# Kernel optimization log

Measured on AMD Instinct MI355X. Metric: run time of the kernel, lower is better.

Reference implementation:

```python
import jax, jax.numpy as jnp
import numpy as np

D_MODEL = 2048
N_HEADS = 16
HEAD_DIM = D_MODEL // N_HEADS  # 128
BASE = 10000.0
NEG = -1e9


def _rope_tables(seq_len, dtype=jnp.float32):
    # inv_freq over even dims of head_dim, emb = cat(freqs, freqs)
    inv_freq = 1.0 / (BASE ** (jnp.arange(0, HEAD_DIM, 2, dtype=jnp.float32) / HEAD_DIM))
    t = jnp.arange(seq_len, dtype=jnp.float32)
    freqs = jnp.einsum('i,j->ij', t, inv_freq)          # [S, hd/2]
    emb = jnp.concatenate([freqs, freqs], axis=-1)       # [S, hd]
    return jnp.cos(emb).astype(dtype)[None, None], jnp.sin(emb).astype(dtype)[None, None]


def _rotate_half(x):
    # Faithful to source: rotary_ndims == head_dim, so x2 is empty and this returns x.
    x1, x2 = x[..., :HEAD_DIM], x[..., HEAD_DIM:]
    return jnp.concatenate([-x2, x1], axis=-1)


def setup_inputs() -> dict:
    key = jax.random.key(0)
    ks = jax.random.split(key, 5)
    B, S = 2, 2048
    x = jax.random.normal(ks[0], (B, S, D_MODEL), dtype=jnp.float32)
    # additive causal mask [1,1,S,S]
    causal = jnp.tril(jnp.ones((S, S), dtype=bool))
    attention_mask = jnp.where(causal, 0.0, NEG).astype(jnp.float32)[None, None]
    scale = 1.0 / np.sqrt(D_MODEL)
    Wq = jax.random.normal(ks[1], (D_MODEL, D_MODEL), dtype=jnp.float32) * scale
    Wk = jax.random.normal(ks[2], (D_MODEL, D_MODEL), dtype=jnp.float32) * scale
    Wv = jax.random.normal(ks[3], (D_MODEL, D_MODEL), dtype=jnp.float32) * scale
    Wd = jax.random.normal(ks[4], (D_MODEL, D_MODEL), dtype=jnp.float32) * scale
    return {"x": x, "attention_mask": attention_mask, "Wq": Wq, "Wk": Wk, "Wv": Wv, "Wd": Wd}


def reference(x, attention_mask, Wq, Wk, Wv, Wd):
    B, S, _ = x.shape
    # torch Linear: y = x @ W.T  (weights stored [out, in])
    def proj(W):
        y = jnp.einsum('bsd,ed->bse', x, W)
        return y.reshape(B, S, N_HEADS, HEAD_DIM).transpose(0, 2, 1, 3)  # [B,H,S,hd]
    q, k, v = proj(Wq), proj(Wk), proj(Wv)
    cos, sin = _rope_tables(S, x.dtype)
    q = q * cos + _rotate_half(q) * sin
    k = k * cos + _rotate_half(k) * sin
    scores = jnp.einsum('bhqd,bhkd->bhqk', q, k) / jnp.sqrt(jnp.float32(HEAD_DIM)).astype(x.dtype)
    scores = scores + attention_mask
    attn = jax.nn.softmax(scores, axis=-1)
    out = jnp.einsum('bhqk,bhkd->bhqd', attn, v)
    out = out.transpose(0, 2, 1, 3).reshape(B, S, D_MODEL)
    return jnp.einsum('bse,de->bsd', out, Wd)
```

## Files before the change

### kernel.cpp

```cpp
#include <hip/hip_runtime.h>
#include <stdint.h>

#define DM   2048
#define NH   16
#define HD   128
#define BB   2
#define SS   2048
#define MM   (BB*SS)
#define KK   2048
#define NQKV (3*DM)

#define LOG2E  1.4426950408889634f
#define SCALE  0.08838834764831845f

using bf16x8 = __attribute__((ext_vector_type(8))) __bf16;
using f32x4  = __attribute__((ext_vector_type(4))) float;
typedef unsigned short u16;
typedef unsigned int   u32;

__device__ __forceinline__ u16 f2bf(float f) {
  u32 u = __float_as_uint(f);
  u32 r = (u + 0x7FFFu + ((u >> 16) & 1u)) >> 16;
  return (u16)r;
}

__device__ __forceinline__ void load_lds16(const void* g, void* l) {
  __builtin_amdgcn_global_load_lds(
      (__attribute__((address_space(1))) void*)(g),
      (__attribute__((address_space(3))) void*)(l), 16, 0, 0);
}

__global__ void cast_f32_bf16(const float* __restrict__ s, u16* __restrict__ d, int n) {
  int i = (blockIdx.x * blockDim.x + threadIdx.x) * 4;
  if (i < n) {
    float4 f = *(const float4*)(s + i);
    u32 lo = (u32)f2bf(f.x) | ((u32)f2bf(f.y) << 16);
    u32 hi = (u32)f2bf(f.z) | ((u32)f2bf(f.w) << 16);
    *(uint2*)(d + i) = make_uint2(lo, hi);
  }
}

__global__ void rope_fct(float* __restrict__ f) {
  int i = blockIdx.x * blockDim.x + threadIdx.x;
  if (i < SS * 128) {
    int s = i >> 7, j = i & 127;
    double inv = pow(10000.0, -(double)(j & 63) / 64.0);
    float ang = (float)s * (float)inv;
    float sn, cs;
    sincosf(ang, &sn, &cs);
    f[i] = cs + sn;
  }
}


__device__ __forceinline__ void stage_unit(const u16* __restrict__ G, int rowbase,
                                           int kbase, u16* lds, int tid) {
#pragma unroll
  for (int i = 0; i < 2; i++) {
    int s = i * 512 + tid;
    int r = s >> 3, c = s & 7;
    load_lds16(G + (size_t)(rowbase + r) * KK + kbase + ((c ^ (r & 7)) * 8),
               (char*)lds + (size_t)s * 16);
  }
}

#define GEMM_MAIN_LOOP(EXTRA_LAST)                                              \
  const int tid = threadIdx.x;                                                  \
  const int wid = tid >> 6, lane = tid & 63, ln = lane & 15, quad = lane >> 4;  \
  const int wm = wid >> 2, wn = wid & 3;                                        \
  const int m0 = blockIdx.x * 256, n0 = blockIdx.y * 128;                       \
  const f32x4 fz = {0.f, 0.f, 0.f, 0.f};                                        \
  f32x4 acc[8][2];                                                              \
  _Pragma("unroll") for (int mi = 0; mi < 8; mi++)                              \
    _Pragma("unroll") for (int ni = 0; ni < 2; ni++) acc[mi][ni] = fz;          \
  int aRow[8], bRow[2];                                                         \
  _Pragma("unroll") for (int mi = 0; mi < 8; mi++)                              \
    aRow[mi] = ((mi < 4) ? (wm * 64 + mi * 16)                                  \
                         : (128 + wm * 64 + (mi - 4) * 16)) + ln;               \
  _Pragma("unroll") for (int ni = 0; ni < 2; ni++)                              \
    bRow[ni] = wn * 32 + ni * 16 + ln;                                          \
                        \
  stage_unit(Bm, n0, 0, LB[0], tid);                                            \
  stage_unit(A, m0, 0, LA[0], tid);                                             \
  stage_unit(A, m0 + 128, 0, LA[0] + 128 * 64, tid);                            \
  const int nT = KK / 64;                                                       \
  for (int t = 0; t < nT; t++) {                                                \
    const int cur = t & 1;                                                      \
    const u16* At = LA[cur];                                                    \
    const u16* Bt = LB[cur];                                                    \
    u16* Ax = LA[cur ^ 1];                                                      \
    u16* Bx = LB[cur ^ 1];                                                      \
    const int kn = (t + 1) * 64;                                                \
    const bool nl = (t + 1 < nT);                                               \
    bf16x8 aF[2][4], bF[2][2];                                                  \
                                    \
    __asm__ __volatile__("s_waitcnt vmcnt(2)" ::: "memory");                    \
    __asm__ __volatile__("s_barrier" ::: "memory");                             \
    _Pragma("unroll") for (int kk = 0; kk < 2; kk++) {                          \
      _Pragma("unroll") for (int mi = 0; mi < 4; mi++)                          \
        aF[kk][mi] = *(const bf16x8*)&At[aRow[mi] * 64 +                        \
                      (((kk * 4 + quad) ^ (aRow[mi] & 7)) * 8)];                \
      _Pragma("unroll") for (int ni = 0; ni < 2; ni++)                          \
        bF[kk][ni] = *(const bf16x8*)&Bt[bRow[ni] * 64 +                        \
                      (((kk * 4 + quad) ^ (bRow[ni] & 7)) * 8)];                \
    }                                                                           \
    if (nl) stage_unit(Bm, n0, kn, Bx, tid);                                    \
    __asm__ __volatile__("s_waitcnt lgkmcnt(0)" ::: "memory");                  \
    __builtin_amdgcn_sched_barrier(0);                                          \
    __builtin_amdgcn_s_setprio(1);                                              \
    _Pragma("unroll") for (int kk = 0; kk < 2; kk++)                            \
      _Pragma("unroll") for (int mi = 0; mi < 4; mi++)                          \
        _Pragma("unroll") for (int ni = 0; ni < 2; ni++)                        \
          acc[mi][ni] = __builtin_amdgcn_mfma_f32_16x16x32_bf16(                \
              aF[kk][mi], bF[kk][ni], acc[mi][ni], 0, 0, 0);                    \
    __builtin_amdgcn_s_setprio(0);                                              \
    __builtin_amdgcn_sched_barrier(0);                                          \
                                  \
    if (nl) { __asm__ __volatile__("s_waitcnt vmcnt(2)" ::: "memory"); }        \
    else    { __asm__ __volatile__("s_waitcnt vmcnt(0)" ::: "memory"); }        \
    __asm__ __volatile__("s_barrier" ::: "memory");                             \
    _Pragma("unroll") for (int kk = 0; kk < 2; kk++)                            \
      _Pragma("unroll") for (int mi = 0; mi < 4; mi++)                          \
        aF[kk][mi] = *(const bf16x8*)&At[aRow[4 + mi] * 64 +                    \
                      (((kk * 4 + quad) ^ (aRow[4 + mi] & 7)) * 8)];            \
    if (nl) {                                                                   \
      stage_unit(A, m0, kn, Ax, tid);                                           \
      stage_unit(A, m0 + 128, kn, Ax + 128 * 64, tid);                          \
    }                                                                           \
    __asm__ __volatile__("s_waitcnt lgkmcnt(0)" ::: "memory");                  \
    __builtin_amdgcn_sched_barrier(0);                                          \
    __builtin_amdgcn_s_setprio(1);                                              \
    _Pragma("unroll") for (int kk = 0; kk < 2; kk++)                            \
      _Pragma("unroll") for (int mi = 0; mi < 4; mi++)                          \
        _Pragma("unroll") for (int ni = 0; ni < 2; ni++)                        \
          acc[4 + mi][ni] = __builtin_amdgcn_mfma_f32_16x16x32_bf16(            \
              aF[kk][mi], bF[kk][ni], acc[4 + mi][ni], 0, 0, 0);                \
    __builtin_amdgcn_s_setprio(0);                                              \
    __builtin_amdgcn_sched_barrier(0);                                          \
    (void)0; EXTRA_LAST                                                         \
  }

__global__ __launch_bounds__(512, 2)
void gemm_qkv_rope(const u16* __restrict__ A, const u16* __restrict__ Bm,
                   u16* __restrict__ qo, u16* __restrict__ ko, u16* __restrict__ vo,
                   const float* __restrict__ fct) {
  __shared__ __align__(16) u16 LA[2][256 * 64];
  __shared__ __align__(16) u16 LB[2][128 * 64];
  GEMM_MAIN_LOOP()

  const int tensor = n0 >> 11;
  const int h = (n0 & 2047) >> 7;
  if (tensor < 2) {
    u16* dst = (tensor == 0) ? qo : ko;
#pragma unroll
    for (int mi = 0; mi < 8; mi++) {
      int rowM = (mi < 4) ? (wm * 64 + mi * 16) : (128 + wm * 64 + (mi - 4) * 16);
#pragma unroll
      for (int r = 0; r < 4; r++) {
        int m = m0 + rowM + quad * 4 + r;
        int b = m >> 11, s = m & 2047;
        const float* fr = fct + s * 128;
#pragma unroll
        for (int ni = 0; ni < 2; ni++) {
          int j = wn * 32 + ni * 16 + ln;
          dst[((size_t)(b * NH + h) * SS + s) * HD + j] = f2bf(acc[mi][ni][r] * fr[j]);
        }
      }
    }
  } else {
    __syncthreads();
    u16* Tr = (u16*)LA;
    const int b = m0 >> 11, s0 = m0 & 2047;
#pragma unroll
    for (int mi = 0; mi < 8; mi++) {
      int rowM = (mi < 4) ? (wm * 64 + mi * 16) : (128 + wm * 64 + (mi - 4) * 16);
#pragma unroll
      for (int ni = 0; ni < 2; ni++) {
        int hd = wn * 32 + ni * 16 + ln;
#pragma unroll
        for (int r = 0; r < 4; r++) {
          int srel = rowM + quad * 4 + r;
          int ch = srel >> 3;
          Tr[hd * 256 + ((ch ^ (hd & 31)) * 8) + (srel & 7)] = f2bf(acc[mi][ni][r]);
        }
      }
    }
    __syncthreads();
#pragma unroll
    for (int it = 0; it < 8; it++) {
      int slot = it * 512 + tid;
      int hd = slot >> 5, c8 = slot & 31;
      uint4 val = *(const uint4*)&Tr[hd * 256 + ((c8 ^ (hd & 31)) * 8)];
      *(uint4*)(vo + ((size_t)(b * NH + h) * HD + hd) * SS + s0 + c8 * 8) = val;
    }
  }
}

__global__ __launch_bounds__(512, 2)
void gemm_out(const u16* __restrict__ A, const u16* __restrict__ Bm,
              float* __restrict__ C) {
  __shared__ __align__(16) u16 LA[2][256 * 64];
  __shared__ __align__(16) u16 LB[2][128 * 64];
  GEMM_MAIN_LOOP()

#pragma unroll
  for (int mi = 0; mi < 8; mi++) {
    int rowM = (mi < 4) ? (wm * 64 + mi * 16) : (128 + wm * 64 + (mi - 4) * 16);
#pragma unroll
    for (int r = 0; r < 4; r++) {
      int m = m0 + rowM + quad * 4 + r;
#pragma unroll
      for (int ni = 0; ni < 2; ni++)
        C[(size_t)m * DM + n0 + wn * 32 + ni * 16 + ln] = acc[mi][ni][r];
    }
  }
}

__global__ __launch_bounds__(256, 2)
void flash_attn(const u16* __restrict__ q, const u16* __restrict__ k,
                const u16* __restrict__ v, u16* __restrict__ o) {
  __shared__ __align__(16) u16 Ps[64 * 64];
  __shared__ __align__(16) u16 Ks[2][64 * 128];
  __shared__ __align__(16) u16 Vs[2][128 * 64];
  const int tid = threadIdx.x;
  const int w = tid >> 6, lane = tid & 63, ln = lane & 15, quad = lane >> 4;
  const int hh = blockIdx.y, b = blockIdx.z;
  const size_t bh = (size_t)b * NH + hh;
  const u16* Kg = k + bh * SS * HD;
  const u16* Vg = v + bh * HD * SS;

  for (int half = 0; half < 2; half++) {
    const int T = half ? (31 - (int)blockIdx.x) : (int)blockIdx.x;
    const u16* Qg = q + bh * SS * HD + (size_t)T * 64 * HD;

    bf16x8 qf[4];
#pragma unroll
    for (int kc = 0; kc < 4; kc++)
      qf[kc] = *(const bf16x8*)(Qg + (size_t)(w * 16 + ln) * HD + (kc * 4 + quad) * 8);

    __syncthreads();

#pragma unroll
    for (int i = 0; i < 4; i++) {
      int slot = i * 256 + tid;
      int r = slot >> 4, c = (slot & 15) ^ (r & 7);
      load_lds16(Kg + (size_t)r * HD + c * 8, (char*)Ks[0] + slot * 16);
    }
#pragma unroll
    for (int i = 0; i < 4; i++) {
      int slot = i * 256 + tid;
      int r = slot >> 3, c = (slot & 7) ^ (r & 7);
      load_lds16(Vg + (size_t)r * SS + c * 8, (char*)Vs[0] + slot * 16);
    }

    const f32x4 fz = {0.f, 0.f, 0.f, 0.f};
    float m_s[4], l_s[4];
    f32x4 accO[8];
#pragma unroll
    for (int r = 0; r < 4; r++) { m_s[r] = -1e30f; l_s[r] = 0.f; }
#pragma unroll
    for (int nt = 0; nt < 8; nt++) accO[nt] = fz;

    const int nkt = T + 1;
    const int qrb = T * 64 + w * 16;

    for (int kt = 0; kt < nkt; kt++) {
      const int cur = kt & 1;
      const int k0 = kt * 64;
      __asm__ __volatile__("s_waitcnt vmcnt(0)" ::: "memory");
      __syncthreads();
      if (kt + 1 < nkt) {
        const int kn = k0 + 64;
#pragma unroll
        for (int i = 0; i < 4; i++) {
          int slot = i * 256 + tid;
          int r = slot >> 4, c = (slot & 15) ^ (r & 7);
          load_lds16(Kg + (size_t)(kn + r) * HD + c * 8, (char*)Ks[cur ^ 1] + slot * 16);
        }
#pragma unroll
        for (int i = 0; i < 4; i++) {
          int slot = i * 256 + tid;
          int r = slot >> 3, c = (slot & 7) ^ (r & 7);
          load_lds16(Vg + (size_t)r * SS + kn + c * 8, (char*)Vs[cur ^ 1] + slot * 16);
        }
      }

      f32x4 sc[4];
#pragma unroll
      for (int nt = 0; nt < 4; nt++) sc[nt] = fz;
#pragma unroll
      for (int kc = 0; kc < 4; kc++)
#pragma unroll
        for (int nt = 0; nt < 4; nt++) {
          bf16x8 bf = *(const bf16x8*)&Ks[cur][(nt * 16 + ln) * 128 + (((kc * 4 + quad) ^ (ln & 7)) * 8)];
          sc[nt] = __builtin_amdgcn_mfma_f32_16x16x32_bf16(qf[kc], bf, sc[nt], 0, 0, 0);
        }

      const bool partial = (kt == T);
#pragma unroll
      for (int nt = 0; nt < 4; nt++)
#pragma unroll
        for (int r = 0; r < 4; r++) {
          float val = sc[nt][r] * SCALE;
          if (partial && (k0 + nt * 16 + ln > qrb + quad * 4 + r)) val = -1e9f;
          sc[nt][r] = val;
        }

#pragma unroll
      for (int r = 0; r < 4; r++) {
        float mx = fmaxf(fmaxf(sc[0][r], sc[1][r]), fmaxf(sc[2][r], sc[3][r]));
#pragma unroll
        for (int off = 1; off < 16; off <<= 1) mx = fmaxf(mx, __shfl_xor(mx, off));
        float mnew = fmaxf(m_s[r], mx);
        float alpha = exp2f((m_s[r] - mnew) * LOG2E);
        float rs = 0.f;
#pragma unroll
        for (int nt = 0; nt < 4; nt++) {
          float p = exp2f((sc[nt][r] - mnew) * LOG2E);
          sc[nt][r] = p;
          rs += p;
        }
#pragma unroll
        for (int off = 1; off < 16; off <<= 1) rs += __shfl_xor(rs, off);
        l_s[r] = l_s[r] * alpha + rs;
        m_s[r] = mnew;
#pragma unroll
        for (int nt = 0; nt < 8; nt++) accO[nt][r] *= alpha;
      }

#pragma unroll
      for (int nt = 0; nt < 4; nt++)
#pragma unroll
        for (int r = 0; r < 4; r++) {
          int rr = w * 16 + quad * 4 + r;
          int j = nt * 16 + ln;
          Ps[rr * 64 + (((j >> 3) ^ (rr & 7)) * 8) + (j & 7)] = f2bf(sc[nt][r]);
        }
      __asm__ __volatile__("s_waitcnt lgkmcnt(0)" ::: "memory");

      bf16x8 pf[2];
#pragma unroll
      for (int kc = 0; kc < 2; kc++) {
        int rp = w * 16 + ln;
        pf[kc] = *(const bf16x8*)&Ps[rp * 64 + (((kc * 4 + quad) ^ (ln & 7)) * 8)];
      }

#pragma unroll
      for (int kc = 0; kc < 2; kc++)
#pragma unroll
        for (int nt = 0; nt < 8; nt++) {
          bf16x8 vf = *(const bf16x8*)&Vs[cur][(nt * 16 + ln) * 64 + (((kc * 4 + quad) ^ (ln & 7)) * 8)];
          accO[nt] = __builtin_amdgcn_mfma_f32_16x16x32_bf16(pf[kc], vf, accO[nt], 0, 0, 0);
        }
    }

#pragma unroll
    for (int r = 0; r < 4; r++) {
      float ilv = 1.f / l_s[r];
      int srow = T * 64 + w * 16 + quad * 4 + r;
      size_t base = ((size_t)b * SS + srow) * DM + hh * HD;
#pragma unroll
      for (int nt = 0; nt < 8; nt++)
        o[base + nt * 16 + ln] = f2bf(accO[nt][r] * ilv);
    }
  }
}

extern "C" void kernel_launch(void* const* d_in, const int* in_sizes, int n_in,
                              void* d_out, int out_size, void* d_ws, size_t ws_size,
                              hipStream_t stream) {
  (void)in_sizes; (void)n_in; (void)out_size; (void)ws_size;
  const float* x  = (const float*)d_in[0];
  const float* Wq = (const float*)d_in[2];
  const float* Wk = (const float*)d_in[3];
  const float* Wv = (const float*)d_in[4];
  const float* Wd = (const float*)d_in[5];

  char* ws = (char*)d_ws;
  u16* xb   = (u16*)(ws);
  u16* aob  = xb;
  u16* wqkv = (u16*)(ws + 16777216ull);
  float* fct = (float*)(ws + 41943040ull);
  u16* wdb  = (u16*)(ws + 41943040ull);
  u16* qb   = (u16*)(ws + 50331648ull);
  u16* kb   = (u16*)(ws + 67108864ull);
  u16* vtb  = (u16*)(ws + 83886080ull);

  cast_f32_bf16<<<8192, 256, 0, stream>>>(x,  xb, MM * KK);
  cast_f32_bf16<<<4096, 256, 0, stream>>>(Wq, wqkv,                   DM * KK);
  cast_f32_bf16<<<4096, 256, 0, stream>>>(Wk, wqkv + (size_t)DM*KK,   DM * KK);
  cast_f32_bf16<<<4096, 256, 0, stream>>>(Wv, wqkv + (size_t)2*DM*KK, DM * KK);
  rope_fct<<<1024, 256, 0, stream>>>(fct);

  gemm_qkv_rope<<<dim3(MM / 256, NQKV / 128), 512, 0, stream>>>(xb, wqkv, qb, kb, vtb, fct);

  cast_f32_bf16<<<4096, 256, 0, stream>>>(Wd, wdb, DM * KK);

  flash_attn<<<dim3(16, NH, BB), 256, 0, stream>>>(qb, kb, vtb, aob);
  gemm_out<<<dim3(MM / 256, DM / 128), 512, 0, stream>>>(aob, wdb, (float*)d_out);
}
```

Before: 400.9 us.

## Transpose GEMM block tile to 128x256 with split B-staging pipeline

Switches the shared GEMM macro from a 256(M)x128(N) block tile to 128(M)x256(N), so each block covers two heads of output columns. LDS is repacked into one flat buffer, and the half-step pipeline now splits the B tile instead of the A tile, with the wait counts adjusted to match. The QKV epilogue gains per-column head indexing, and the V transpose path uses a new swizzle. The tile area and LDS footprint stay the same; the intent is a different stage/compute interleaving and wider output rows, at the risk of changed global load balance and wait-count correctness.

New measurement: 391.0 us. 1.03x faster.

```diff
diff --git a/kernel.cpp b/kernel.cpp
--- a/kernel.cpp
+++ b/kernel.cpp
@@ -64,36 +64,37 @@
   }
 }
 
-#define GEMM_MAIN_LOOP(EXTRA_LAST)                                              \
+#define COLN(ni) (((ni) < 2) ? (wn * 32 + (ni) * 16) : (128 + wn * 32 + ((ni) - 2) * 16))
+
+#define GEMM_MAIN_LOOP                                                          \
   const int tid = threadIdx.x;                                                  \
   const int wid = tid >> 6, lane = tid & 63, ln = lane & 15, quad = lane >> 4;  \
   const int wm = wid >> 2, wn = wid & 3;                                        \
-  const int m0 = blockIdx.x * 256, n0 = blockIdx.y * 128;                       \
+  const int m0 = blockIdx.x * 128, n0 = blockIdx.y * 256;                       \
   const f32x4 fz = {0.f, 0.f, 0.f, 0.f};                                        \
-  f32x4 acc[8][2];                                                              \
-  _Pragma("unroll") for (int mi = 0; mi < 8; mi++)                              \
-    _Pragma("unroll") for (int ni = 0; ni < 2; ni++) acc[mi][ni] = fz;          \
-  int aRow[8], bRow[2];                                                         \
-  _Pragma("unroll") for (int mi = 0; mi < 8; mi++)                              \
-    aRow[mi] = ((mi < 4) ? (wm * 64 + mi * 16)                                  \
-                         : (128 + wm * 64 + (mi - 4) * 16)) + ln;               \
-  _Pragma("unroll") for (int ni = 0; ni < 2; ni++)                              \
-    bRow[ni] = wn * 32 + ni * 16 + ln;                                          \
-                        \
-  stage_unit(Bm, n0, 0, LB[0], tid);                                            \
-  stage_unit(A, m0, 0, LA[0], tid);                                             \
-  stage_unit(A, m0 + 128, 0, LA[0] + 128 * 64, tid);                            \
+  f32x4 acc[4][4];                                                              \
+  _Pragma("unroll") for (int mi = 0; mi < 4; mi++)                              \
+    _Pragma("unroll") for (int ni = 0; ni < 4; ni++) acc[mi][ni] = fz;          \
+  int aRow[4], bRow[4];                                                         \
+  _Pragma("unroll") for (int mi = 0; mi < 4; mi++)                              \
+    aRow[mi] = wm * 64 + mi * 16 + ln;                                          \
+  _Pragma("unroll") for (int ni = 0; ni < 4; ni++)                              \
+    bRow[ni] = COLN(ni) + ln;                                                   \
+                            \
+  stage_unit(A, m0, 0, Sh, tid);                                                \
+  stage_unit(Bm, n0, 0, Sh + 16384, tid);                                       \
+  stage_unit(Bm, n0 + 128, 0, Sh + 16384 + 8192, tid);                          \
   const int nT = KK / 64;                                                       \
   for (int t = 0; t < nT; t++) {                                                \
     const int cur = t & 1;                                                      \
-    const u16* At = LA[cur];                                                    \
-    const u16* Bt = LB[cur];                                                    \
-    u16* Ax = LA[cur ^ 1];                                                      \
-    u16* Bx = LB[cur ^ 1];                                                      \
+    const u16* At = Sh + cur * 8192;                                            \
+    const u16* Bt = Sh + 16384 + cur * 16384;                                   \
+    u16* Ax = Sh + (cur ^ 1) * 8192;                                            \
+    u16* Bx = Sh + 16384 + (cur ^ 1) * 16384;                                   \
     const int kn = (t + 1) * 64;                                                \
     const bool nl = (t + 1 < nT);                                               \
     bf16x8 aF[2][4], bF[2][2];                                                  \
-                                    \
+                              \
     __asm__ __volatile__("s_waitcnt vmcnt(2)" ::: "memory");                    \
     __asm__ __volatile__("s_barrier" ::: "memory");                             \
     _Pragma("unroll") for (int kk = 0; kk < 2; kk++) {                          \
@@ -104,7 +105,10 @@
         bF[kk][ni] = *(const bf16x8*)&Bt[bRow[ni] * 64 +                        \
                       (((kk * 4 + quad) ^ (bRow[ni] & 7)) * 8)];                \
     }                                                                           \
-    if (nl) stage_unit(Bm, n0, kn, Bx, tid);                                    \
+    if (nl) {                                                                   \
+      stage_unit(A, m0, kn, Ax, tid);                                           \
+      stage_unit(Bm, n0, kn, Bx, tid);                                          \
+    }                                                                           \
     __asm__ __volatile__("s_waitcnt lgkmcnt(0)" ::: "memory");                  \
     __builtin_amdgcn_sched_barrier(0);                                          \
     __builtin_amdgcn_s_setprio(1);                                              \
@@ -115,73 +119,70 @@
               aF[kk][mi], bF[kk][ni], acc[mi][ni], 0, 0, 0);                    \
     __builtin_amdgcn_s_setprio(0);                                              \
     __builtin_amdgcn_sched_barrier(0);                                          \
-                                  \
-    if (nl) { __asm__ __volatile__("s_waitcnt vmcnt(2)" ::: "memory"); }        \
+                         \
+    if (nl) { __asm__ __volatile__("s_waitcnt vmcnt(4)" ::: "memory"); }        \
     else    { __asm__ __volatile__("s_waitcnt vmcnt(0)" ::: "memory"); }        \
     __asm__ __volatile__("s_barrier" ::: "memory");                             \
     _Pragma("unroll") for (int kk = 0; kk < 2; kk++)                            \
-      _Pragma("unroll") for (int mi = 0; mi < 4; mi++)                          \
-        aF[kk][mi] = *(const bf16x8*)&At[aRow[4 + mi] * 64 +                    \
-                      (((kk * 4 + quad) ^ (aRow[4 + mi] & 7)) * 8)];            \
-    if (nl) {                                                                   \
-      stage_unit(A, m0, kn, Ax, tid);                                           \
-      stage_unit(A, m0 + 128, kn, Ax + 128 * 64, tid);                          \
-    }                                                                           \
+      _Pragma("unroll") for (int ni = 0; ni < 2; ni++)                          \
+        bF[kk][ni] = *(const bf16x8*)&Bt[bRow[2 + ni] * 64 +                    \
+                      (((kk * 4 + quad) ^ (bRow[2 + ni] & 7)) * 8)];            \
+    if (nl) stage_unit(Bm, n0 + 128, kn, Bx + 8192, tid);                       \
     __asm__ __volatile__("s_waitcnt lgkmcnt(0)" ::: "memory");                  \
     __builtin_amdgcn_sched_barrier(0);                                          \
     __builtin_amdgcn_s_setprio(1);                                              \
     _Pragma("unroll") for (int kk = 0; kk < 2; kk++)                            \
       _Pragma("unroll") for (int mi = 0; mi < 4; mi++)                          \
         _Pragma("unroll") for (int ni = 0; ni < 2; ni++)                        \
-          acc[4 + mi][ni] = __builtin_amdgcn_mfma_f32_16x16x32_bf16(            \
-              aF[kk][mi], bF[kk][ni], acc[4 + mi][ni], 0, 0, 0);                \
+          acc[mi][2 + ni] = __builtin_amdgcn_mfma_f32_16x16x32_bf16(            \
+              aF[kk][mi], bF[kk][ni], acc[mi][2 + ni], 0, 0, 0);                \
     __builtin_amdgcn_s_setprio(0);                                              \
     __builtin_amdgcn_sched_barrier(0);                                          \
-    (void)0; EXTRA_LAST                                                         \
   }
 
 __global__ __launch_bounds__(512, 2)
 void gemm_qkv_rope(const u16* __restrict__ A, const u16* __restrict__ Bm,
                    u16* __restrict__ qo, u16* __restrict__ ko, u16* __restrict__ vo,
                    const float* __restrict__ fct) {
-  __shared__ __align__(16) u16 LA[2][256 * 64];
-  __shared__ __align__(16) u16 LB[2][128 * 64];
-  GEMM_MAIN_LOOP()
+  __shared__ __align__(16) u16 Sh[49152];
+  GEMM_MAIN_LOOP
 
   const int tensor = n0 >> 11;
-  const int h = (n0 & 2047) >> 7;
+  const int h0 = (n0 & 2047) >> 7;
   if (tensor < 2) {
     u16* dst = (tensor == 0) ? qo : ko;
 #pragma unroll
-    for (int mi = 0; mi < 8; mi++) {
-      int rowM = (mi < 4) ? (wm * 64 + mi * 16) : (128 + wm * 64 + (mi - 4) * 16);
+    for (int mi = 0; mi < 4; mi++) {
+      int rowM = wm * 64 + mi * 16;
 #pragma unroll
       for (int r = 0; r < 4; r++) {
         int m = m0 + rowM + quad * 4 + r;
         int b = m >> 11, s = m & 2047;
         const float* fr = fct + s * 128;
 #pragma unroll
-        for (int ni = 0; ni < 2; ni++) {
-          int j = wn * 32 + ni * 16 + ln;
+        for (int ni = 0; ni < 4; ni++) {
+          int colN = COLN(ni) + ln;
+          int h = h0 + (colN >> 7);
+          int j = colN & 127;
           dst[((size_t)(b * NH + h) * SS + s) * HD + j] = f2bf(acc[mi][ni][r] * fr[j]);
         }
       }
     }
   } else {
     __syncthreads();
-    u16* Tr = (u16*)LA;
+    u16* Tr = Sh;
     const int b = m0 >> 11, s0 = m0 & 2047;
 #pragma unroll
-    for (int mi = 0; mi < 8; mi++) {
-      int rowM = (mi < 4) ? (wm * 64 + mi * 16) : (128 + wm * 64 + (mi - 4) * 16);
-#pragma unroll
-      for (int ni = 0; ni < 2; ni++) {
-        int hd = wn * 32 + ni * 16 + ln;
+    for (int mi = 0; mi < 4; mi++) {
+      int rowM = wm * 64 + mi * 16;
+#pragma unroll
+      for (int ni = 0; ni < 4; ni++) {
+        int colN = COLN(ni) + ln;
 #pragma unroll
         for (int r = 0; r < 4; r++) {
           int srel = rowM + quad * 4 + r;
           int ch = srel >> 3;
-          Tr[hd * 256 + ((ch ^ (hd & 31)) * 8) + (srel & 7)] = f2bf(acc[mi][ni][r]);
+          Tr[colN * 128 + ((ch ^ (colN & 15)) * 8) + (srel & 7)] = f2bf(acc[mi][ni][r]);
         }
       }
     }
@@ -189,8 +190,9 @@
 #pragma unroll
     for (int it = 0; it < 8; it++) {
       int slot = it * 512 + tid;
-      int hd = slot >> 5, c8 = slot & 31;
-      uint4 val = *(const uint4*)&Tr[hd * 256 + ((c8 ^ (hd & 31)) * 8)];
+      int nloc = slot >> 4, c8 = slot & 15;
+      uint4 val = *(const uint4*)&Tr[nloc * 128 + ((c8 ^ (nloc & 15)) * 8)];
+      int h = h0 + (nloc >> 7), hd = nloc & 127;
       *(uint4*)(vo + ((size_t)(b * NH + h) * HD + hd) * SS + s0 + c8 * 8) = val;
     }
   }
@@ -199,19 +201,20 @@
 __global__ __launch_bounds__(512, 2)
 void gemm_out(const u16* __restrict__ A, const u16* __restrict__ Bm,
               float* __restrict__ C) {
-  __shared__ __align__(16) u16 LA[2][256 * 64];
-  __shared__ __align__(16) u16 LB[2][128 * 64];
-  GEMM_MAIN_LOOP()
-
-#pragma unroll
-  for (int mi = 0; mi < 8; mi++) {
-    int rowM = (mi < 4) ? (wm * 64 + mi * 16) : (128 + wm * 64 + (mi - 4) * 16);
+  __shared__ __align__(16) u16 Sh[49152];
+  GEMM_MAIN_LOOP
+
+#pragma unroll
+  for (int mi = 0; mi < 4; mi++) {
+    int rowM = wm * 64 + mi * 16;
 #pragma unroll
     for (int r = 0; r < 4; r++) {
       int m = m0 + rowM + quad * 4 + r;
 #pragma unroll
-      for (int ni = 0; ni < 2; ni++)
-        C[(size_t)m * DM + n0 + wn * 32 + ni * 16 + ln] = acc[mi][ni][r];
+      for (int ni = 0; ni < 4; ni++) {
+        int colN = COLN(ni) + ln;
+        C[(size_t)m * DM + n0 + colN] = acc[mi][ni][r];
+      }
     }
   }
 }
@@ -392,10 +395,10 @@
   cast_f32_bf16<<<4096, 256, 0, stream>>>(Wv, wqkv + (size_t)2*DM*KK, DM * KK);
   rope_fct<<<1024, 256, 0, stream>>>(fct);
 
-  gemm_qkv_rope<<<dim3(MM / 256, NQKV / 128), 512, 0, stream>>>(xb, wqkv, qb, kb, vtb, fct);
+  gemm_qkv_rope<<<dim3(MM / 128, NQKV / 256), 512, 0, stream>>>(xb, wqkv, qb, kb, vtb, fct);
 
   cast_f32_bf16<<<4096, 256, 0, stream>>>(Wd, wdb, DM * KK);
 
   flash_attn<<<dim3(16, NH, BB), 256, 0, stream>>>(qb, kb, vtb, aob);
-  gemm_out<<<dim3(MM / 256, DM / 128), 512, 0, stream>>>(aob, wdb, (float*)d_out);
-}
+  gemm_out<<<dim3(MM / 128, DM / 256), 512, 0, stream>>>(aob, wdb, (float*)d_out);
+}
```
